# Kernel optimization log

Hardware: AMD Instinct MI355X
Metric: run time of the kernel (lower is better)

Reference implementation:

```python
import jax, jax.numpy as jnp
import numpy as np

H, B, C, R, L, A, NEAR = 4, 8, 64, 64, 2048, 8, 2
EPS = 1e-5

def setup_inputs() -> dict:
    key = jax.random.key(0)
    ks = jax.random.split(key, 16)
    d = {}
    d['inputs'] = jax.random.normal(ks[0], (H, B, C, L), jnp.float32)
    d['hidden'] = jax.random.normal(ks[1], (B, R, L), jnp.float32)
    # per-head spatial attention 1x1 convs (no bias)
    d['key_w'] = jax.random.normal(ks[2], (H, R, C), jnp.float32) * 0.05
    d['value_w'] = jax.random.normal(ks[3], (H, C, C), jnp.float32) * 0.05
    # channel attention (1x1 convs with bias)
    HC = H * C
    d['ca_w1'] = jax.random.normal(ks[4], (A, HC + R), jnp.float32) * 0.05
    d['ca_b1'] = jnp.zeros((A,), jnp.float32)
    d['ca_w2'] = jax.random.normal(ks[5], (HC, A), jnp.float32) * 0.05
    d['ca_b2'] = jnp.zeros((HC,), jnp.float32)
    # projection: conv3(no bias) -> BN -> relu -> conv3(no bias) -> BN -> relu
    d['pw1'] = jax.random.normal(ks[6], (R, HC, 3), jnp.float32) * 0.02
    d['bn1_g'] = jnp.ones((R,), jnp.float32)
    d['bn1_b'] = jnp.zeros((R,), jnp.float32)
    d['bn1_m'] = jnp.zeros((R,), jnp.float32)
    d['bn1_v'] = jnp.ones((R,), jnp.float32)
    d['pw2'] = jax.random.normal(ks[7], (R, R, 3), jnp.float32) * 0.02
    d['bn2_g'] = jnp.ones((R,), jnp.float32)
    d['bn2_b'] = jnp.zeros((R,), jnp.float32)
    d['bn2_m'] = jnp.zeros((R,), jnp.float32)
    d['bn2_v'] = jnp.ones((R,), jnp.float32)
    return d

def _bn(x, g, b, m, v):
    # eval-mode BatchNorm1d over channel dim of [B,C,L]
    inv = g / jnp.sqrt(v + EPS)
    return x * inv[None, :, None] + (b - m * inv)[None, :, None]

def _conv3(x, w):
    # [B,Cin,L] x [Cout,Cin,3] -> [B,Cout,L], padding=1
    return jax.lax.conv_general_dilated(x, w, (1,), 'SAME',
                                        dimension_numbers=('NCH', 'OIH', 'NCH'))

def reference(inputs, hidden, key_w, value_w, ca_w1, ca_b1, ca_w2, ca_b2,
              pw1, bn1_g, bn1_b, bn1_m, bn1_v, pw2, bn2_g, bn2_b, bn2_m, bn2_v):
    scale = 1.0 / jnp.sqrt(jnp.float32(R))
    # spatial attention, vectorized over heads
    k = jnp.einsum('hrc,hbcl->hbrl', key_w, inputs)      # keys
    v = jnp.einsum('hoc,hbcl->hbol', value_w, inputs)    # values
    q = hidden * scale                                   # [B,R,L]
    attn = jnp.einsum('brl,hbrm->hblm', q, k)            # [H,B,L,L]
    idx = jnp.arange(L)
    band = (jnp.abs(idx[:, None] - idx[None, :]) <= NEAR).astype(attn.dtype)
    attn = jax.nn.softmax(attn * band, axis=-1)          # multiplicative mask then softmax (faithful)
    val = jnp.einsum('hbcl,hblm->hbcm', v, attn)
    enc = inputs + val                                   # dropout in eval = identity
    x = jnp.transpose(enc, (1, 0, 2, 3)).reshape(B, H * C, L)  # concat heads on channel
    # channel attention gating
    cat = jnp.concatenate([x, hidden], axis=1)           # [B,HC+R,L]
    a = jax.nn.relu(jnp.einsum('oc,bcl->bol', ca_w1, cat) + ca_b1[None, :, None])
    gate = jax.nn.sigmoid(jnp.einsum('oa,bal->bol', ca_w2, a) + ca_b2[None, :, None])
    x = x * gate
    # projection
    y = jax.nn.relu(_bn(_conv3(x, pw1), bn1_g, bn1_b, bn1_m, bn1_v))
    y = jax.nn.relu(_bn(_conv3(y, pw2), bn2_g, bn2_b, bn2_m, bn2_v))
    return y
```

## Files before the change

kernel.cpp:

```cpp
#include <hip/hip_runtime.h>
#include <hip/hip_bf16.h>
#include <math.h>

#define HH 4
#define BB 8
#define CC 64
#define RR 64
#define LL 2048
#define AA 8
#define HC 256
#define EPS 1e-5f
#define CHP 266

typedef unsigned short ushort_t;
typedef __attribute__((ext_vector_type(8))) short short8;
typedef __attribute__((ext_vector_type(4))) float f32x4;

static __device__ __forceinline__ ushort_t f2bf(float x) {
    unsigned u = __float_as_uint(x);
    unsigned r = (u + 0x7FFF + ((u >> 16) & 1)) >> 16;
    return (ushort_t)r;
}
static __device__ __forceinline__ float bf2f(ushort_t h) {
    return __uint_as_float(((unsigned)h) << 16);
}
static __device__ __forceinline__ void pack8(const float* p, short8& hi, short8& lo) {
    float4 x0 = *(const float4*)p;
    float4 x1 = *(const float4*)(p + 4);
    float xs[8] = {x0.x, x0.y, x0.z, x0.w, x1.x, x1.y, x1.z, x1.w};
#pragma unroll
    for (int e = 0; e < 8; ++e) {
        ushort_t h = f2bf(xs[e]);
        hi[e] = (short)h;
        lo[e] = (short)f2bf(xs[e] - bf2f(h));
    }
}

__global__ __launch_bounds__(256) void kABC(const float* __restrict__ inp,
                                            const float* __restrict__ kw,
                                            const float* __restrict__ vw,
                                            const float* __restrict__ hidden,
                                            float* __restrict__ V,
                                            float* __restrict__ U,
                                            float* __restrict__ W,
                                            float* __restrict__ Spart,
                                            const float* __restrict__ pw1,
                                            const float* __restrict__ g1,
                                            const float* __restrict__ m1,
                                            const float* __restrict__ v1,
                                            const float* __restrict__ bb1,
                                            const float* __restrict__ pw2,
                                            const float* __restrict__ g2,
                                            const float* __restrict__ m2,
                                            const float* __restrict__ v2,
                                            const float* __restrict__ bb2,
                                            const float* __restrict__ w1ca,
                                            ushort_t* __restrict__ wEb,
                                            ushort_t* __restrict__ wFb,
                                            float* __restrict__ biasE,
                                            float* __restrict__ biasF,
                                            float* __restrict__ w1T) {
    if (blockIdx.x == 32) {
        int tid = blockIdx.y * 256 + threadIdx.x;
        const int stride = 32 * 256;
        for (int idx = tid; idx < 4 * 24 * 64 * 8; idx += stride) {
            int j = idx & 7, lane = (idx >> 3) & 63, t2 = idx >> 9;
            int ks = t2 % 24, rg = t2 / 24;
            int r = rg * 16 + (lane & 15);
            int k = ks * 32 + (lane >> 4) * 8 + j;
            int tap = k >> 8, ch = k & 255;
            float inv = g1[r] * rsqrtf(v1[r] + EPS);
            wEb[idx] = f2bf(pw1[(r * 256 + ch) * 3 + tap] * inv);
        }
        for (int idx = tid; idx < 4 * 6 * 64 * 8; idx += stride) {
            int j = idx & 7, lane = (idx >> 3) & 63, t2 = idx >> 9;
            int ks = t2 % 6, rg = t2 / 6;
            int r = rg * 16 + (lane & 15);
            int k = ks * 32 + (lane >> 4) * 8 + j;
            int tap = k >> 6, c = k & 63;
            float inv = g2[r] * rsqrtf(v2[r] + EPS);
            wFb[idx] = f2bf(pw2[(r * 64 + c) * 3 + tap] * inv);
        }
        for (int idx = tid; idx < 320 * 8; idx += stride)
            w1T[idx] = w1ca[(idx & 7) * 320 + (idx >> 3)];
        if (tid < 64) {
            float inv1 = g1[tid] * rsqrtf(v1[tid] + EPS);
            biasE[tid] = bb1[tid] - m1[tid] * inv1;
            float inv2 = g2[tid] * rsqrtf(v2[tid] + EPS);
            biasF[tid] = bb2[tid] - m2[tid] * inv2;
        }
        return;
    }
    int hb = blockIdx.x;
    int h = hb >> 3;
    int b = hb & 7;
    int l0 = blockIdx.y * 64;
    __shared__ __align__(16) char shbuf[2 * 80 * 72 * 2];
    ushort_t (*xsT)[80][72] = (ushort_t (*)[80][72])shbuf;
    float (*k_s)[76] = (float (*)[76])shbuf;
    __shared__ float partial[4][64][5];
    __shared__ float u_s[64];
    __shared__ float red_s[64];
    int t = threadIdx.x;
    int lane = t & 63, wv = t >> 6;
    int a = lane & 15, kg = lane >> 4;
    short8 ah[2][2], al[2][2];
    {
        const float* kwh = kw + h * 4096;
        const float* vwh = vw + h * 4096;
#pragma unroll
        for (int rtl = 0; rtl < 2; ++rtl) {
            int rt = wv * 2 + rtl;
            int row = rt * 16 + a;
            const float* base = (rt < 4) ? (kwh + row * 64) : (vwh + (row - 64) * 64);
#pragma unroll
            for (int ks = 0; ks < 2; ++ks)
                pack8(base + ks * 32 + kg * 8, ah[rtl][ks], al[rtl][ks]);
        }
    }
    {
        float xv[20];
#pragma unroll
        for (int it = 0; it < 20; ++it) {
            int idx = t + it * 256;
            int ch = idx / 80, j = idx % 80;
            int l = l0 - 2 + j;
            xv[it] = (j < 68 && l >= 0 && l < LL)
                   ? inp[(size_t)(hb * 64 + ch) * LL + l] : 0.f;
        }
#pragma unroll
        for (int it = 0; it < 20; ++it) {
            int idx = t + it * 256;
            int ch = idx / 80, j = idx % 80;
            ushort_t hi = f2bf(xv[it]);
            xsT[0][j][ch] = hi;
            xsT[1][j][ch] = f2bf(xv[it] - bf2f(hi));
        }
    }
    __syncthreads();
    f32x4 acc[2][5] = {};
#pragma unroll
    for (int ks = 0; ks < 2; ++ks) {
#pragma unroll
        for (int ct = 0; ct < 5; ++ct) {
            short8 bhf = *(const short8*)&xsT[0][ct * 16 + a][ks * 32 + kg * 8];
            short8 blf = *(const short8*)&xsT[1][ct * 16 + a][ks * 32 + kg * 8];
#pragma unroll
            for (int rtl = 0; rtl < 2; ++rtl) {
                acc[rtl][ct] = __builtin_amdgcn_mfma_f32_16x16x32_bf16(ah[rtl][ks], bhf, acc[rtl][ct], 0, 0, 0);
                acc[rtl][ct] = __builtin_amdgcn_mfma_f32_16x16x32_bf16(ah[rtl][ks], blf, acc[rtl][ct], 0, 0, 0);
                acc[rtl][ct] = __builtin_amdgcn_mfma_f32_16x16x32_bf16(al[rtl][ks], bhf, acc[rtl][ct], 0, 0, 0);
            }
        }
    }
    __syncthreads();
#pragma unroll
    for (int rtl = 0; rtl < 2; ++rtl) {
        int rt = wv * 2 + rtl;
#pragma unroll
        for (int ct = 0; ct < 5; ++ct) {
            int j = ct * 16 + a;
#pragma unroll
            for (int reg = 0; reg < 4; ++reg) {
                int row = rt * 16 + kg * 4 + reg;
                float val = acc[rtl][ct][reg];
                if (rt < 4) {
                    if (j < 68) k_s[row][j] = val;
                } else {
                    if (j >= 2 && j < 66)
                        V[(size_t)(hb * 64 + row - 64) * LL + l0 - 2 + j] = val;
                }
            }
        }
    }
    __syncthreads();
    {
        float acc5[5] = {};
        const float* hp = hidden + (size_t)(b * 64 + wv * 16) * LL + l0 + lane;
#pragma unroll 4
        for (int i = 0; i < 16; ++i) {
            float hh = hp[(size_t)i * LL];
            int r = wv * 16 + i;
            acc5[0] += hh * k_s[r][lane];
            acc5[1] += hh * k_s[r][lane + 1];
            acc5[2] += hh * k_s[r][lane + 2];
            acc5[3] += hh * k_s[r][lane + 3];
            acc5[4] += hh * k_s[r][lane + 4];
        }
#pragma unroll
        for (int d = 0; d < 5; ++d) partial[wv][lane][d] = acc5[d];
    }
    __syncthreads();
    if (t < 64) {
        int l = l0 + t;
        float raw[5];
        float mx = 0.f;
        int nv = 0;
#pragma unroll
        for (int d = 0; d < 5; ++d) {
            float s = partial[0][t][d] + partial[1][t][d]
                    + partial[2][t][d] + partial[3][t][d];
            int m = l + d - 2;
            bool valid = (m >= 0 && m < LL);
            raw[d] = valid ? s * 0.125f : -1e30f;
            if (valid) { nv++; mx = fmaxf(mx, raw[d]); }
        }
        float e0 = __expf(-mx);
        float Z = (float)(LL - nv) * e0;
        float w[5];
#pragma unroll
        for (int d = 0; d < 5; ++d) {
            float e = (raw[d] > -1e29f) ? __expf(raw[d] - mx) : 0.f;
            w[d] = e;
            Z += e;
        }
        float inv = 1.f / Z;
        float u = e0 * inv;
        U[(size_t)hb * LL + l] = u;
#pragma unroll
        for (int d = 0; d < 5; ++d) W[((size_t)hb * LL + l) * 5 + d] = w[d] * inv;
        u_s[t] = u;
    }
    __syncthreads();
    if (wv >= 2) {
#pragma unroll
        for (int rtl = 0; rtl < 2; ++rtl) {
#pragma unroll
            for (int reg = 0; reg < 4; ++reg) {
                float s = 0.f;
#pragma unroll
                for (int ct = 0; ct < 5; ++ct) {
                    int j = ct * 16 + a;
                    if (j >= 2 && j < 66) s += acc[rtl][ct][reg] * u_s[j - 2];
                }
                s += __shfl_xor(s, 1);
                s += __shfl_xor(s, 2);
                s += __shfl_xor(s, 4);
                s += __shfl_xor(s, 8);
                if (a == 0) {
                    int c = (wv * 2 + rtl - 4) * 16 + kg * 4 + reg;
                    red_s[c] = s;
                }
            }
        }
    }
    __syncthreads();
    if (t < 64)
        Spart[((size_t)hb * 32 + blockIdx.y) * 64 + t] = red_s[t];
}

__global__ __launch_bounds__(512) void kD(const float* __restrict__ inp,
                                          const float* __restrict__ hidden,
                                          const float* __restrict__ V,
                                          const float* __restrict__ U,
                                          const float* __restrict__ W,
                                          const float* __restrict__ Spart,
                                          const float* __restrict__ w1T,
                                          const float* __restrict__ b1,
                                          const float* __restrict__ w2,
                                          const float* __restrict__ b2,
                                          float* __restrict__ XG) {
    int b = blockIdx.x;
    int m0 = blockIdx.y * 64;
    __shared__ float Vt[64][68];
    __shared__ float dw_s[4][68][5];
    __shared__ float S2_s[2][256];
    __shared__ float partial[8][64][9];
    int t = threadIdx.x;
    int m = t & 63;
    int wv = t >> 6;
    for (int idx = t; idx < 4 * 68; idx += 512) {
        int h = idx / 68, j = idx % 68;
        int l = m0 - 2 + j;
        int hb = h * 8 + b;
        if (l >= 0 && l < LL) {
            float u = U[(size_t)hb * LL + l];
            const float* wp = &W[((size_t)hb * LL + l) * 5];
#pragma unroll
            for (int d = 0; d < 5; ++d) dw_s[h][j][d] = wp[d] - u;
        } else {
#pragma unroll
            for (int d = 0; d < 5; ++d) dw_s[h][j][d] = 0.f;
        }
    }
    {
        int qh = t >> 8;
        int ci = t & 255;
        int hb = (ci >> 6) * 8 + b;
        float s = 0.f;
#pragma unroll
        for (int q = 0; q < 16; ++q)
            s += Spart[((size_t)hb * 32 + qh * 16 + q) * 64 + (ci & 63)];
        S2_s[qh][ci] = s;
    }
    float xr[4][8];
#pragma unroll
    for (int h = 0; h < 4; ++h) {
        __syncthreads();
        int hb8 = h * 8 + b;
        for (int idx = t; idx < 64 * 68; idx += 512) {
            int c = idx / 68, j = idx % 68;
            int l = m0 - 2 + j;
            Vt[c][j] = (l >= 0 && l < LL) ? V[(size_t)(hb8 * 64 + c) * LL + l] : 0.f;
        }
        __syncthreads();
        float dwv[5];
#pragma unroll
        for (int d = 0; d < 5; ++d) dwv[d] = dw_s[h][m + 4 - d][d];
#pragma unroll
        for (int cc = 0; cc < 8; ++cc) {
            int c = wv * 8 + cc;
            int ch = h * 64 + c;
            float v0 = Vt[c][m], v1 = Vt[c][m + 1], v2 = Vt[c][m + 2];
            float v3 = Vt[c][m + 3], v4 = Vt[c][m + 4];
            float val = S2_s[0][ch] + S2_s[1][ch]
                      + v4 * dwv[0] + v3 * dwv[1] + v2 * dwv[2]
                      + v1 * dwv[3] + v0 * dwv[4];
            xr[h][cc] = inp[(size_t)(hb8 * 64 + c) * LL + m0 + m] + val;
        }
    }
    float acc2[8] = {};
    int cb = __builtin_amdgcn_readfirstlane(wv * 8);
#pragma unroll
    for (int h = 0; h < 4; ++h) {
#pragma unroll
        for (int cc = 0; cc < 8; ++cc) {
            const float* wp = w1T + (h * 64 + cb + cc) * 8;
            float xv = xr[h][cc];
#pragma unroll
            for (int o = 0; o < 8; ++o) acc2[o] += wp[o] * xv;
        }
    }
#pragma unroll
    for (int i = 0; i < 8; ++i) {
        const float* wp = w1T + (256 + cb + i) * 8;
        float xv = hidden[(size_t)(b * 64 + cb + i) * LL + m0 + m];
#pragma unroll
        for (int o = 0; o < 8; ++o) acc2[o] += wp[o] * xv;
    }
#pragma unroll
    for (int o = 0; o < 8; ++o) partial[wv][m][o] = acc2[o];
    __syncthreads();
    float a[8];
#pragma unroll
    for (int o = 0; o < 8; ++o) {
        float v = b1[o];
#pragma unroll
        for (int p = 0; p < 8; ++p) v += partial[p][m][o];
        a[o] = fmaxf(v, 0.f);
    }
#pragma unroll
    for (int h = 0; h < 4; ++h) {
#pragma unroll
        for (int cc = 0; cc < 8; ++cc) {
            int ch = h * 64 + cb + cc;
            const float* wp = w2 + ch * 8;
            float g = b2[ch];
#pragma unroll
            for (int o = 0; o < 8; ++o) g += wp[o] * a[o];
            float gate = 1.f / (1.f + __expf(-g));
            XG[(size_t)(b * 256 + ch) * LL + m0 + m] = xr[h][cc] * gate;
        }
    }
}

__global__ __launch_bounds__(256) void kConvM(const float* __restrict__ XG,
                                              const ushort_t* __restrict__ wEb,
                                              const float* __restrict__ biasE,
                                              float* __restrict__ Y1) {
    int b = blockIdx.x;
    int l0 = blockIdx.y * 32;
    __shared__ ushort_t xts[2][34][CHP];
    __shared__ float bias_s[64];
    int t = threadIdx.x;
    if (t < 64) bias_s[t] = biasE[t];
    for (int q = t; q < 34 * 64; q += 256) {
        int row = q % 34;
        int ch0 = (q / 34) * 4;
        int l = l0 - 1 + row;
        bool v = (l >= 0 && l < LL);
        unsigned hp[2], lp[2];
#pragma unroll
        for (int p = 0; p < 2; ++p) {
            unsigned h2 = 0, l2 = 0;
#pragma unroll
            for (int i = 0; i < 2; ++i) {
                int ch = ch0 + p * 2 + i;
                float x = v ? XG[(size_t)(b * 256 + ch) * LL + l] : 0.f;
                ushort_t hi = f2bf(x);
                ushort_t lo = f2bf(x - bf2f(hi));
                h2 |= ((unsigned)hi) << (16 * i);
                l2 |= ((unsigned)lo) << (16 * i);
            }
            hp[p] = h2; lp[p] = l2;
        }
        *(unsigned*)&xts[0][row][ch0] = hp[0];
        *(unsigned*)&xts[0][row][ch0 + 2] = hp[1];
        *(unsigned*)&xts[1][row][ch0] = lp[0];
        *(unsigned*)&xts[1][row][ch0 + 2] = lp[1];
    }
    __syncthreads();
    int lane = t & 63;
    int wid = t >> 6;
    int wm = wid & 1, wn = wid >> 1;
    int a = lane & 15;
    int kg = lane >> 4;
    f32x4 acc[2] = {};
    union U8 { unsigned u[4]; short8 s; };
#pragma unroll 4
    for (int ks = 0; ks < 24; ++ks) {
        int tap = ks >> 3;
        int ch0 = ((ks & 7) << 5) + (kg << 3);
        short8 afr[2];
#pragma unroll
        for (int tr = 0; tr < 2; ++tr) {
            const ushort_t* ap = wEb + ((((size_t)(wm * 2 + tr) * 24 + ks) * 64 + lane) << 3);
            afr[tr] = *(const short8*)ap;
        }
        int row = wn * 16 + a + tap;
        const ushort_t* xh = &xts[0][row][ch0];
        const ushort_t* xl = &xts[1][row][ch0];
        U8 bh, bl;
#pragma unroll
        for (int qq = 0; qq < 4; ++qq) {
            bh.u[qq] = *(const unsigned*)(xh + 2 * qq);
            bl.u[qq] = *(const unsigned*)(xl + 2 * qq);
        }
#pragma unroll
        for (int tr = 0; tr < 2; ++tr) {
            acc[tr] = __builtin_amdgcn_mfma_f32_16x16x32_bf16(afr[tr], bh.s, acc[tr], 0, 0, 0);
            acc[tr] = __builtin_amdgcn_mfma_f32_16x16x32_bf16(afr[tr], bl.s, acc[tr], 0, 0, 0);
        }
    }
#pragma unroll
    for (int tr = 0; tr < 2; ++tr) {
        int m = wn * 16 + a;
#pragma unroll
        for (int reg = 0; reg < 4; ++reg) {
            int r = wm * 32 + tr * 16 + kg * 4 + reg;
            float y = acc[tr][reg] + bias_s[r];
            Y1[(size_t)(b * 64 + r) * LL + l0 + m] = fmaxf(y, 0.f);
        }
    }
}

__global__ __launch_bounds__(256) void kCM2(const float* __restrict__ Y1,
                                            const ushort_t* __restrict__ wFb,
                                            const float* __restrict__ biasF,
                                            float* __restrict__ out) {
    int b = blockIdx.x;
    int l0 = blockIdx.y * 32;
    __shared__ ushort_t yts[2][34][70];
    __shared__ float bias_s[64];
    int t = threadIdx.x;
    if (t < 64) bias_s[t] = biasF[t];
    for (int q = t; q < 34 * 16; q += 256) {
        int row = q % 34;
        int c0 = (q / 34) * 4;
        int l = l0 - 1 + row;
        bool v = (l >= 0 && l < LL);
        unsigned hp[2], lp[2];
#pragma unroll
        for (int p = 0; p < 2; ++p) {
            unsigned h2 = 0, l2 = 0;
#pragma unroll
            for (int i = 0; i < 2; ++i) {
                int c = c0 + p * 2 + i;
                float x = v ? Y1[(size_t)(b * 64 + c) * LL + l] : 0.f;
                ushort_t hi = f2bf(x);
                ushort_t lo = f2bf(x - bf2f(hi));
                h2 |= ((unsigned)hi) << (16 * i);
                l2 |= ((unsigned)lo) << (16 * i);
            }
            hp[p] = h2; lp[p] = l2;
        }
        *(unsigned*)&yts[0][row][c0] = hp[0];
        *(unsigned*)&yts[0][row][c0 + 2] = hp[1];
        *(unsigned*)&yts[1][row][c0] = lp[0];
        *(unsigned*)&yts[1][row][c0 + 2] = lp[1];
    }
    __syncthreads();
    int lane = t & 63;
    int wid = t >> 6;
    int wm = wid & 1, wn = wid >> 1;
    int a = lane & 15;
    int kg = lane >> 4;
    f32x4 acc[2] = {};
    union U8 { unsigned u[4]; short8 s; };
#pragma unroll
    for (int ks = 0; ks < 6; ++ks) {
        int tap = ks >> 1;
        int c0 = ((ks & 1) << 5) + (kg << 3);
        short8 afr[2];
#pragma unroll
        for (int tr = 0; tr < 2; ++tr) {
            const ushort_t* ap = wFb + ((((size_t)(wm * 2 + tr) * 6 + ks) * 64 + lane) << 3);
            afr[tr] = *(const short8*)ap;
        }
        int s = wn * 16 + a + tap;
        const ushort_t* yh = &yts[0][s][c0];
        const ushort_t* yl = &yts[1][s][c0];
        U8 bh, bl;
#pragma unroll
        for (int qq = 0; qq < 4; ++qq) {
            bh.u[qq] = *(const unsigned*)(yh + 2 * qq);
            bl.u[qq] = *(const unsigned*)(yl + 2 * qq);
        }
#pragma unroll
        for (int tr = 0; tr < 2; ++tr) {
            acc[tr] = __builtin_amdgcn_mfma_f32_16x16x32_bf16(afr[tr], bh.s, acc[tr], 0, 0, 0);
            acc[tr] = __builtin_amdgcn_mfma_f32_16x16x32_bf16(afr[tr], bl.s, acc[tr], 0, 0, 0);
        }
    }
#pragma unroll
    for (int tr = 0; tr < 2; ++tr) {
        int m = wn * 16 + a;
#pragma unroll
        for (int reg = 0; reg < 4; ++reg) {
            int r = wm * 32 + tr * 16 + kg * 4 + reg;
            float y = acc[tr][reg] + bias_s[r];
            out[(size_t)(b * 64 + r) * LL + l0 + m] = fmaxf(y, 0.f);
        }
    }
}

extern "C" void kernel_launch(void* const* d_in, const int* in_sizes, int n_in,
                              void* d_out, int out_size, void* d_ws, size_t ws_size,
                              hipStream_t stream) {
    (void)in_sizes; (void)n_in; (void)out_size; (void)ws_size;
    const float* inp    = (const float*)d_in[0];
    const float* hidden = (const float*)d_in[1];
    const float* key_w  = (const float*)d_in[2];
    const float* value_w= (const float*)d_in[3];
    const float* ca_w1  = (const float*)d_in[4];
    const float* ca_b1  = (const float*)d_in[5];
    const float* ca_w2  = (const float*)d_in[6];
    const float* ca_b2  = (const float*)d_in[7];
    const float* pw1    = (const float*)d_in[8];
    const float* bn1_g  = (const float*)d_in[9];
    const float* bn1_b  = (const float*)d_in[10];
    const float* bn1_m  = (const float*)d_in[11];
    const float* bn1_v  = (const float*)d_in[12];
    const float* pw2    = (const float*)d_in[13];
    const float* bn2_g  = (const float*)d_in[14];
    const float* bn2_b  = (const float*)d_in[15];
    const float* bn2_m  = (const float*)d_in[16];
    const float* bn2_v  = (const float*)d_in[17];

    float* ws = (float*)d_ws;
    const size_t KV = (size_t)HH * BB * CC * LL;
    float* XG = ws;
    float* V = ws + KV;
    float* U = ws + 2 * KV;
    float* W = U + (size_t)HH * BB * LL;
    float* Spart = W + (size_t)HH * BB * LL * 5;
    float* w1T   = Spart + 65536;
    float* biasE = w1T + 2560;
    float* biasF = biasE + 64;
    ushort_t* wEb = (ushort_t*)(biasF + 64);
    ushort_t* wFb = (ushort_t*)(biasF + 64 + 24576);
    float* Y1 = V;

    kABC<<<dim3(33, 32), 256, 0, stream>>>(inp, key_w, value_w, hidden,
                                           V, U, W, Spart,
                                           pw1, bn1_g, bn1_m, bn1_v, bn1_b,
                                           pw2, bn2_g, bn2_m, bn2_v, bn2_b,
                                           ca_w1, wEb, wFb, biasE, biasF, w1T);
    kD<<<dim3(BB, LL / 64), 512, 0, stream>>>(inp, hidden, V, U, W, Spart,
                                              w1T, ca_b1, ca_w2, ca_b2, XG);
    kConvM<<<dim3(BB, 64), 256, 0, stream>>>(XG, wEb, biasE, Y1);
    kCM2<<<dim3(BB, 64), 256, 0, stream>>>(Y1, wFb, biasF, (float*)d_out);
}
```

Measured before the change: 77.53 us.

## Compute banded attention correction in kABC and pass XC to kD

kABC now widens its tile halo so it can compute the banded softmax weights for neighbouring positions itself. It applies the local 5-tap value correction in-block and writes one XC tensor, instead of writing V, U and W for kD to reload and recombine. kD then just adds inp, XC and the per-channel sum, dropping its shared-memory V staging and per-head syncs. The cost is extra halo work and score recomputation in kABC (68 vs 64 positions, 72-wide input load).

```diff
diff --git a/kernel.cpp b/kernel.cpp
--- a/kernel.cpp
+++ b/kernel.cpp
@@ -40,9 +40,7 @@
                                             const float* __restrict__ kw,
                                             const float* __restrict__ vw,
                                             const float* __restrict__ hidden,
-                                            float* __restrict__ V,
-                                            float* __restrict__ U,
-                                            float* __restrict__ W,
+                                            float* __restrict__ XC,
                                             float* __restrict__ Spart,
                                             const float* __restrict__ pw1,
                                             const float* __restrict__ g1,
@@ -98,8 +96,9 @@
     __shared__ __align__(16) char shbuf[2 * 80 * 72 * 2];
     ushort_t (*xsT)[80][72] = (ushort_t (*)[80][72])shbuf;
     float (*k_s)[76] = (float (*)[76])shbuf;
-    __shared__ float partial[4][64][5];
-    __shared__ float u_s[64];
+    __shared__ float partial[4][68][5];
+    __shared__ float dw_s[68][5];
+    __shared__ float u_s68[68];
     __shared__ float red_s[64];
     int t = threadIdx.x;
     int lane = t & 63, wv = t >> 6;
@@ -124,8 +123,8 @@
         for (int it = 0; it < 20; ++it) {
             int idx = t + it * 256;
             int ch = idx / 80, j = idx % 80;
-            int l = l0 - 2 + j;
-            xv[it] = (j < 68 && l >= 0 && l < LL)
+            int l = l0 - 4 + j;
+            xv[it] = (j < 72 && l >= 0 && l < LL)
                    ? inp[(size_t)(hb * 64 + ch) * LL + l] : 0.f;
         }
 #pragma unroll
@@ -157,18 +156,14 @@
 #pragma unroll
     for (int rtl = 0; rtl < 2; ++rtl) {
         int rt = wv * 2 + rtl;
-#pragma unroll
-        for (int ct = 0; ct < 5; ++ct) {
-            int j = ct * 16 + a;
-#pragma unroll
-            for (int reg = 0; reg < 4; ++reg) {
-                int row = rt * 16 + kg * 4 + reg;
-                float val = acc[rtl][ct][reg];
-                if (rt < 4) {
-                    if (j < 68) k_s[row][j] = val;
-                } else {
-                    if (j >= 2 && j < 66)
-                        V[(size_t)(hb * 64 + row - 64) * LL + l0 - 2 + j] = val;
+        if (rt < 4) {
+#pragma unroll
+            for (int ct = 0; ct < 5; ++ct) {
+                int j = ct * 16 + a;
+#pragma unroll
+                for (int reg = 0; reg < 4; ++reg) {
+                    int row = rt * 16 + kg * 4 + reg;
+                    if (j < 72) k_s[row][j] = acc[rtl][ct][reg];
                 }
             }
         }
@@ -176,7 +171,9 @@
     __syncthreads();
     {
         float acc5[5] = {};
-        const float* hp = hidden + (size_t)(b * 64 + wv * 16) * LL + l0 + lane;
+        int l = l0 - 2 + lane;
+        int lc = min(max(l, 0), LL - 1);
+        const float* hp = hidden + (size_t)(b * 64 + wv * 16) * LL + lc;
 #pragma unroll 4
         for (int i = 0; i < 16; ++i) {
             float hh = hp[(size_t)i * LL];
@@ -189,71 +186,112 @@
         }
 #pragma unroll
         for (int d = 0; d < 5; ++d) partial[wv][lane][d] = acc5[d];
-    }
-    __syncthreads();
-    if (t < 64) {
-        int l = l0 + t;
-        float raw[5];
-        float mx = 0.f;
-        int nv = 0;
-#pragma unroll
-        for (int d = 0; d < 5; ++d) {
-            float s = partial[0][t][d] + partial[1][t][d]
-                    + partial[2][t][d] + partial[3][t][d];
-            int m = l + d - 2;
-            bool valid = (m >= 0 && m < LL);
-            raw[d] = valid ? s * 0.125f : -1e30f;
-            if (valid) { nv++; mx = fmaxf(mx, raw[d]); }
-        }
-        float e0 = __expf(-mx);
-        float Z = (float)(LL - nv) * e0;
-        float w[5];
-#pragma unroll
-        for (int d = 0; d < 5; ++d) {
-            float e = (raw[d] > -1e29f) ? __expf(raw[d] - mx) : 0.f;
-            w[d] = e;
-            Z += e;
-        }
-        float inv = 1.f / Z;
-        float u = e0 * inv;
-        U[(size_t)hb * LL + l] = u;
-#pragma unroll
-        for (int d = 0; d < 5; ++d) W[((size_t)hb * LL + l) * 5 + d] = w[d] * inv;
-        u_s[t] = u;
+        if (lane < 4) {
+            int li2 = 64 + lane;
+            int lb = l0 - 2 + li2;
+            int lcb = min(max(lb, 0), LL - 1);
+            float acc5b[5] = {};
+            const float* hpb = hidden + (size_t)(b * 64 + wv * 16) * LL + lcb;
+#pragma unroll 4
+            for (int i = 0; i < 16; ++i) {
+                float hh = hpb[(size_t)i * LL];
+                int r = wv * 16 + i;
+                acc5b[0] += hh * k_s[r][li2];
+                acc5b[1] += hh * k_s[r][li2 + 1];
+                acc5b[2] += hh * k_s[r][li2 + 2];
+                acc5b[3] += hh * k_s[r][li2 + 3];
+                acc5b[4] += hh * k_s[r][li2 + 4];
+            }
+#pragma unroll
+            for (int d = 0; d < 5; ++d) partial[wv][li2][d] = acc5b[d];
+        }
+    }
+    __syncthreads();
+    if (t < 68) {
+        int l = l0 - 2 + t;
+        if (l < 0 || l >= LL) {
+            u_s68[t] = 0.f;
+#pragma unroll
+            for (int d = 0; d < 5; ++d) dw_s[t][d] = 0.f;
+        } else {
+            float raw[5];
+            float mx = 0.f;
+            int nv = 0;
+#pragma unroll
+            for (int d = 0; d < 5; ++d) {
+                float s = partial[0][t][d] + partial[1][t][d]
+                        + partial[2][t][d] + partial[3][t][d];
+                int m = l + d - 2;
+                bool valid = (m >= 0 && m < LL);
+                raw[d] = valid ? s * 0.125f : -1e30f;
+                if (valid) { nv++; mx = fmaxf(mx, raw[d]); }
+            }
+            float e0 = __expf(-mx);
+            float Z = (float)(LL - nv) * e0;
+            float w[5];
+#pragma unroll
+            for (int d = 0; d < 5; ++d) {
+                float e = (raw[d] > -1e29f) ? __expf(raw[d] - mx) : 0.f;
+                w[d] = e;
+                Z += e;
+            }
+            float inv = 1.f / Z;
+            float u = e0 * inv;
+            u_s68[t] = u;
+#pragma unroll
+            for (int d = 0; d < 5; ++d) dw_s[t][d] = w[d] * inv - u;
+        }
     }
     __syncthreads();
     if (wv >= 2) {
 #pragma unroll
         for (int rtl = 0; rtl < 2; ++rtl) {
+            int vr0 = (wv * 2 + rtl - 4) * 16 + kg * 4;
+#pragma unroll
+            for (int ct = 0; ct < 5; ++ct) {
+                int j = ct * 16 + a;
+#pragma unroll
+                for (int reg = 0; reg < 4; ++reg) {
+                    if (j >= 2 && j < 70) k_s[vr0 + reg][j] = acc[rtl][ct][reg];
+                }
+            }
 #pragma unroll
             for (int reg = 0; reg < 4; ++reg) {
                 float s = 0.f;
 #pragma unroll
                 for (int ct = 0; ct < 5; ++ct) {
                     int j = ct * 16 + a;
-                    if (j >= 2 && j < 66) s += acc[rtl][ct][reg] * u_s[j - 2];
+                    if (j >= 4 && j < 68) s += acc[rtl][ct][reg] * u_s68[j - 2];
                 }
                 s += __shfl_xor(s, 1);
                 s += __shfl_xor(s, 2);
                 s += __shfl_xor(s, 4);
                 s += __shfl_xor(s, 8);
-                if (a == 0) {
-                    int c = (wv * 2 + rtl - 4) * 16 + kg * 4 + reg;
-                    red_s[c] = s;
-                }
-            }
-        }
-    }
-    __syncthreads();
+                if (a == 0) red_s[vr0 + reg] = s;
+            }
+        }
+    }
+    __syncthreads();
+    {
+        int mm = t & 63;
+        int cq = t >> 6;
+#pragma unroll
+        for (int it = 0; it < 16; ++it) {
+            int c = it * 4 + cq;
+            float xc = 0.f;
+#pragma unroll
+            for (int o = -2; o <= 2; ++o)
+                xc += k_s[c][mm - o + 4] * dw_s[mm - o + 2][o + 2];
+            XC[(size_t)(hb * 64 + c) * LL + l0 + mm] = xc;
+        }
+    }
     if (t < 64)
         Spart[((size_t)hb * 32 + blockIdx.y) * 64 + t] = red_s[t];
 }
 
 __global__ __launch_bounds__(512) void kD(const float* __restrict__ inp,
                                           const float* __restrict__ hidden,
-                                          const float* __restrict__ V,
-                                          const float* __restrict__ U,
-                                          const float* __restrict__ W,
+                                          const float* __restrict__ XC,
                                           const float* __restrict__ Spart,
                                           const float* __restrict__ w1T,
                                           const float* __restrict__ b1,
@@ -262,65 +300,32 @@
                                           float* __restrict__ XG) {
     int b = blockIdx.x;
     int m0 = blockIdx.y * 64;
-    __shared__ float Vt[64][68];
-    __shared__ float dw_s[4][68][5];
-    __shared__ float S2_s[2][256];
+    __shared__ float S2_s[256];
     __shared__ float partial[8][64][9];
     int t = threadIdx.x;
     int m = t & 63;
     int wv = t >> 6;
-    for (int idx = t; idx < 4 * 68; idx += 512) {
-        int h = idx / 68, j = idx % 68;
-        int l = m0 - 2 + j;
-        int hb = h * 8 + b;
-        if (l >= 0 && l < LL) {
-            float u = U[(size_t)hb * LL + l];
-            const float* wp = &W[((size_t)hb * LL + l) * 5];
-#pragma unroll
-            for (int d = 0; d < 5; ++d) dw_s[h][j][d] = wp[d] - u;
-        } else {
-#pragma unroll
-            for (int d = 0; d < 5; ++d) dw_s[h][j][d] = 0.f;
-        }
-    }
-    {
-        int qh = t >> 8;
-        int ci = t & 255;
-        int hb = (ci >> 6) * 8 + b;
+    if (t < 256) {
+        int hb = (t >> 6) * 8 + b;
         float s = 0.f;
 #pragma unroll
-        for (int q = 0; q < 16; ++q)
-            s += Spart[((size_t)hb * 32 + qh * 16 + q) * 64 + (ci & 63)];
-        S2_s[qh][ci] = s;
-    }
+        for (int q = 0; q < 32; ++q)
+            s += Spart[((size_t)hb * 32 + q) * 64 + (t & 63)];
+        S2_s[t] = s;
+    }
+    __syncthreads();
     float xr[4][8];
+    int cb = __builtin_amdgcn_readfirstlane(wv * 8);
 #pragma unroll
     for (int h = 0; h < 4; ++h) {
-        __syncthreads();
-        int hb8 = h * 8 + b;
-        for (int idx = t; idx < 64 * 68; idx += 512) {
-            int c = idx / 68, j = idx % 68;
-            int l = m0 - 2 + j;
-            Vt[c][j] = (l >= 0 && l < LL) ? V[(size_t)(hb8 * 64 + c) * LL + l] : 0.f;
-        }
-        __syncthreads();
-        float dwv[5];
-#pragma unroll
-        for (int d = 0; d < 5; ++d) dwv[d] = dw_s[h][m + 4 - d][d];
 #pragma unroll
         for (int cc = 0; cc < 8; ++cc) {
-            int c = wv * 8 + cc;
-            int ch = h * 64 + c;
-            float v0 = Vt[c][m], v1 = Vt[c][m + 1], v2 = Vt[c][m + 2];
-            float v3 = Vt[c][m + 3], v4 = Vt[c][m + 4];
-            float val = S2_s[0][ch] + S2_s[1][ch]
-                      + v4 * dwv[0] + v3 * dwv[1] + v2 * dwv[2]
-                      + v1 * dwv[3] + v0 * dwv[4];
-            xr[h][cc] = inp[(size_t)(hb8 * 64 + c) * LL + m0 + m] + val;
+            int c = cb + cc;
+            size_t idx = (size_t)((h * 8 + b) * 64 + c) * LL + m0 + m;
+            xr[h][cc] = inp[idx] + XC[idx] + S2_s[h * 64 + c];
         }
     }
     float acc2[8] = {};
-    int cb = __builtin_amdgcn_readfirstlane(wv * 8);
 #pragma unroll
     for (int h = 0; h < 4; ++h) {
 #pragma unroll
@@ -550,23 +555,21 @@
     float* ws = (float*)d_ws;
     const size_t KV = (size_t)HH * BB * CC * LL;
     float* XG = ws;
-    float* V = ws + KV;
-    float* U = ws + 2 * KV;
-    float* W = U + (size_t)HH * BB * LL;
-    float* Spart = W + (size_t)HH * BB * LL * 5;
+    float* XC = ws + KV;
+    float* Spart = ws + 2 * KV;
     float* w1T   = Spart + 65536;
     float* biasE = w1T + 2560;
     float* biasF = biasE + 64;
     ushort_t* wEb = (ushort_t*)(biasF + 64);
     ushort_t* wFb = (ushort_t*)(biasF + 64 + 24576);
-    float* Y1 = V;
+    float* Y1 = XC;
 
     kABC<<<dim3(33, 32), 256, 0, stream>>>(inp, key_w, value_w, hidden,
-                                           V, U, W, Spart,
+                                           XC, Spart,
                                            pw1, bn1_g, bn1_m, bn1_v, bn1_b,
                                            pw2, bn2_g, bn2_m, bn2_v, bn2_b,
                                            ca_w1, wEb, wFb, biasE, biasF, w1T);
-    kD<<<dim3(BB, LL / 64), 512, 0, stream>>>(inp, hidden, V, U, W, Spart,
+    kD<<<dim3(BB, LL / 64), 512, 0, stream>>>(inp, hidden, XC, Spart,
                                               w1T, ca_b1, ca_w2, ca_b2, XG);
     kConvM<<<dim3(BB, 64), 256, 0, stream>>>(XG, wEb, biasE, Y1);
     kCM2<<<dim3(BB, 64), 256, 0, stream>>>(Y1, wFb, biasF, (float*)d_out);
```

Measured after the change: 65.75 us. 1.18x faster.
